# Optimization experiments

Hardware: AMD Instinct MI355X
Metric: run time of the kernel (lower is better)

Reference implementation:

```python
import jax, jax.numpy as jnp
import numpy as np

INPUT_SIZE = 2048
HIDDEN_SIZE = 4096
NUM_CLASSES = 1000
BATCH = 4096


def setup_inputs() -> dict:
    key = jax.random.key(0)
    kx, k1, k2, k3 = jax.random.split(key, 4)
    x = jax.random.normal(kx, (BATCH, INPUT_SIZE), dtype=jnp.float32)
    w1 = jax.random.normal(k1, (INPUT_SIZE, HIDDEN_SIZE), dtype=jnp.float32) * 0.01
    b1 = jnp.zeros((HIDDEN_SIZE,), dtype=jnp.float32)
    w2 = jax.random.normal(k2, (HIDDEN_SIZE, HIDDEN_SIZE), dtype=jnp.float32) * 0.01
    b2 = jnp.zeros((HIDDEN_SIZE,), dtype=jnp.float32)
    w3 = jax.random.normal(k3, (HIDDEN_SIZE, NUM_CLASSES), dtype=jnp.float32) * 0.01
    b3 = jnp.zeros((NUM_CLASSES,), dtype=jnp.float32)
    return {"x": x, "w1": w1, "b1": b1, "w2": w2, "b2": b2, "w3": w3, "b3": b3}


def reference(x, w1, b1, w2, b2, w3, b3):
    # fused GEMM + bias + ReLU, equivalent to the original Python double-loop matmul
    h1 = jax.nn.relu(x @ w1 + b1)    # [B, H]
    h2 = jax.nn.relu(h1 @ w2 + b2)   # [B, H]
    out = h2 @ w3 + b3               # [B, C]
    return out
```

## Files before the change

kernel.cpp:

```cpp
#include <hip/hip_runtime.h>
#include <hip/hip_bf16.h>

typedef __bf16 bf16x8 __attribute__((ext_vector_type(8)));
typedef __bf16 bf16x4 __attribute__((ext_vector_type(4)));
typedef float floatx4 __attribute__((ext_vector_type(4)));

#define B_    4096
#define IN_   2048
#define HID_  4096
#define NC_   1000
#define NCP_  1024

__device__ __forceinline__ void transpose_cvt_dev(const float* __restrict__ src,
                                                  __bf16* __restrict__ dst,
                                                  int R, int C, int bx, int by,
                                                  float* tile ) {
    const int r0 = bx * 64;
    const int c0 = by * 64;
    const int t  = threadIdx.x;
#pragma unroll
    for (int it = 0; it < 4; ++it) {
        int lin = it * 256 + t;
        int sr = lin >> 4, c4 = lin & 15;
        int cb = c0 + c4 * 4;
        const float* s = src + (size_t)(r0 + sr) * C;
        float4 v;
        if (cb + 3 < C) {
            v = *(const float4*)(s + cb);
        } else {
            v.x = (cb + 0 < C) ? s[cb + 0] : 0.f;
            v.y = (cb + 1 < C) ? s[cb + 1] : 0.f;
            v.z = (cb + 2 < C) ? s[cb + 2] : 0.f;
            v.w = (cb + 3 < C) ? s[cb + 3] : 0.f;
        }
        tile[(c4 * 4 + 0) * 65 + sr] = v.x;
        tile[(c4 * 4 + 1) * 65 + sr] = v.y;
        tile[(c4 * 4 + 2) * 65 + sr] = v.z;
        tile[(c4 * 4 + 3) * 65 + sr] = v.w;
    }
    __syncthreads();
#pragma unroll
    for (int it = 0; it < 2; ++it) {
        int lin = it * 256 + t;
        int dr = lin >> 3, q8 = lin & 7;
        bf16x8 o;
#pragma unroll
        for (int j = 0; j < 8; ++j) o[j] = (__bf16)tile[dr * 65 + q8 * 8 + j];
        *(bf16x8*)(dst + (size_t)(c0 + dr) * R + r0 + q8 * 8) = o;
    }
}

__device__ __forceinline__ void swizzle32x32(int bid, int& bx, int& by) {
    int xcd = bid & 7;
    int q   = bid >> 3;
    by = ((xcd >> 2) << 4) + (q & 15);
    bx = ((xcd & 3) << 3) + (q >> 4);
}

template <bool RELU, bool OUT_BF16>
__device__ __forceinline__ void gemm_core(const __bf16* __restrict__ A,
                                          const __bf16* __restrict__ Bt,
                                          const float* __restrict__ bias,
                                          void* __restrict__ Cv,
                                          int M, int K, int Nstore,
                                          int bx, int by,
                                          __bf16* sA, __bf16* sB) {
    const int tid   = threadIdx.x;
    const int lane  = tid & 63;
    const int wave  = tid >> 6;
    const int wr    = wave >> 1;
    const int wc    = wave & 1;
    const int mBase = by * 128;
    const int nBase = bx * 128;
    const int lr    = lane >> 4;
    const int lc    = lane & 15;

    floatx4 acc[4][4];
#pragma unroll
    for (int i = 0; i < 4; ++i)
#pragma unroll
        for (int j = 0; j < 4; ++j) acc[i][j] = (floatx4)0.f;

    for (int k0 = 0; k0 < K; k0 += 64) {
#pragma unroll
        for (int it = 0; it < 4; ++it) {
            int lin = it * 256 + tid;
            int r   = lin >> 3;
            int kc  = (lin & 7) ^ (r & 7);
            const __bf16* ga = A  + (size_t)(mBase + r) * K + k0 + kc * 8;
            const __bf16* gb = Bt + (size_t)(nBase + r) * K + k0 + kc * 8;
            __builtin_amdgcn_global_load_lds(
                (__attribute__((address_space(1))) void*)ga,
                (__attribute__((address_space(3))) void*)(sA + lin * 8), 16, 0, 0);
            __builtin_amdgcn_global_load_lds(
                (__attribute__((address_space(1))) void*)gb,
                (__attribute__((address_space(3))) void*)(sB + lin * 8), 16, 0, 0);
        }
        __builtin_amdgcn_s_waitcnt(0);
        __syncthreads();

#pragma unroll
        for (int kk = 0; kk < 2; ++kk) {
            const int sw = (kk * 4 + lr) ^ (lc & 7);
            bf16x8 af[4], bfr[4];
#pragma unroll
            for (int i = 0; i < 4; ++i)
                af[i] = *(const bf16x8*)(sA + (wr * 64 + i * 16 + lc) * 64 + sw * 8);
#pragma unroll
            for (int j = 0; j < 4; ++j)
                bfr[j] = *(const bf16x8*)(sB + (wc * 64 + j * 16 + lc) * 64 + sw * 8);
#pragma unroll
            for (int i = 0; i < 4; ++i)
#pragma unroll
                for (int j = 0; j < 4; ++j)
                    acc[i][j] = __builtin_amdgcn_mfma_f32_16x16x32_bf16(af[i], bfr[j], acc[i][j], 0, 0, 0);
        }
        __syncthreads();
    }

#pragma unroll
    for (int j = 0; j < 4; ++j) {
        int col = nBase + wc * 64 + j * 16 + lc;
        if (col < Nstore) {
            float bv = bias[col];
#pragma unroll
            for (int i = 0; i < 4; ++i) {
                int rowb = mBase + wr * 64 + i * 16 + lr * 4;
#pragma unroll
                for (int r = 0; r < 4; ++r) {
                    float v = acc[i][j][r] + bv;
                    if (RELU) v = fmaxf(v, 0.f);
                    if (OUT_BF16)
                        ((__bf16*)Cv)[(size_t)(rowb + r) * Nstore + col] = (__bf16)v;
                    else
                        ((float*)Cv)[(size_t)(rowb + r) * Nstore + col] = v;
                }
            }
        }
    }
}

__global__ __launch_bounds__(256) void prep1(const float* __restrict__ x,
                                             __bf16* __restrict__ xb,
                                             const float* __restrict__ w1,
                                             __bf16* __restrict__ w1t) {
    __shared__ float tile[64 * 65];
    const int b = blockIdx.x;
    if (b < 4096) {
        int i = (b * 256 + (int)threadIdx.x) * 8;
        float4 a = *(const float4*)(x + i);
        float4 c = *(const float4*)(x + i + 4);
        bf16x8 o;
        o[0] = (__bf16)a.x; o[1] = (__bf16)a.y; o[2] = (__bf16)a.z; o[3] = (__bf16)a.w;
        o[4] = (__bf16)c.x; o[5] = (__bf16)c.y; o[6] = (__bf16)c.z; o[7] = (__bf16)c.w;
        *(bf16x8*)(xb + i) = o;
    } else {
        int l = b - 4096;
        transpose_cvt_dev(w1, w1t, IN_, HID_, l & 31, l >> 5, tile);
    }
}

__global__ __launch_bounds__(256, 2) void gemm1_fused(const __bf16* __restrict__ xb,
                                                      const __bf16* __restrict__ w1t,
                                                      const float* __restrict__ b1,
                                                      __bf16* __restrict__ h1,
                                                      const float* __restrict__ w2,
                                                      __bf16* __restrict__ w2t,
                                                      const float* __restrict__ w3,
                                                      __bf16* __restrict__ w3t) {
    __shared__ float smem[8192];
    const int b = blockIdx.x;
    if (b < 1024) {
        __bf16* sA = (__bf16*)smem;
        __bf16* sB = sA + 128 * 64;
        int bx, by;
        swizzle32x32(b, bx, by);
        gemm_core<true, true>(xb, w1t, b1, h1, B_, IN_, HID_, bx, by, sA, sB);
    } else if (b < 5120) {
        int l = b - 1024;
        transpose_cvt_dev(w2, w2t, HID_, HID_, l & 63, l >> 6, smem);
    } else {
        int l = b - 5120;
        transpose_cvt_dev(w3, w3t, HID_, NC_, l & 63, l >> 6, smem);
    }
}

#define QPHASE(pA, pB, qm, qn, ...)                                            \
  {                                                                            \
    bf16x8 af0[4], af1[4], bq0[2], bq1[2];                                     \
    _Pragma("unroll") for (int i_ = 0; i_ < 4; ++i_) {                         \
      const __bf16* ap_ = (pA) + ((wr * 128 + (qm) * 64 + i_ * 16 + lc) * 64); \
      af0[i_] = *(const bf16x8*)(ap_ + ((0 + lr) ^ (lc & 7)) * 8);             \
      af1[i_] = *(const bf16x8*)(ap_ + ((4 + lr) ^ (lc & 7)) * 8);             \
    }                                                                          \
    _Pragma("unroll") for (int j_ = 0; j_ < 2; ++j_) {                         \
      const __bf16* bp_ = (pB) + ((wc * 64 + (qn) * 32 + j_ * 16 + lc) * 64);  \
      bq0[j_] = *(const bf16x8*)(bp_ + ((0 + lr) ^ (lc & 7)) * 8);             \
      bq1[j_] = *(const bf16x8*)(bp_ + ((4 + lr) ^ (lc & 7)) * 8);             \
    }                                                                          \
    __VA_ARGS__;                                                               \
    __builtin_amdgcn_s_barrier();                                              \
    asm volatile("s_waitcnt lgkmcnt(0)" ::: "memory");                         \
    __builtin_amdgcn_sched_barrier(0);                                         \
    __builtin_amdgcn_s_setprio(1);                                             \
    _Pragma("unroll") for (int i_ = 0; i_ < 4; ++i_)                           \
      _Pragma("unroll") for (int j_ = 0; j_ < 2; ++j_) {                       \
        acc[(qm) * 4 + i_][(qn) * 2 + j_] =                                    \
            __builtin_amdgcn_mfma_f32_16x16x32_bf16(                           \
                af0[i_], bq0[j_], acc[(qm) * 4 + i_][(qn) * 2 + j_], 0, 0, 0); \
        acc[(qm) * 4 + i_][(qn) * 2 + j_] =                                    \
            __builtin_amdgcn_mfma_f32_16x16x32_bf16(                           \
                af1[i_], bq1[j_], acc[(qm) * 4 + i_][(qn) * 2 + j_], 0, 0, 0); \
      }                                                                        \
    __builtin_amdgcn_s_setprio(0);                                             \
    __builtin_amdgcn_s_barrier();                                              \
  }

__global__ __launch_bounds__(512, 2) void gemm2_256(const __bf16* __restrict__ A,
                                                    const __bf16* __restrict__ Bt,
                                                    const float* __restrict__ bias,
                                                    __bf16* __restrict__ C) {
    extern __shared__ __bf16 lds[];
    const int K  = HID_;
    const int NT = K / 64;

    const int tid  = threadIdx.x;
    const int lane = tid & 63;
    const int wave = tid >> 6;
    const int wr   = wave >> 2;
    const int wc   = wave & 3;
    const int lr   = lane >> 4;
    const int lc   = lane & 15;

    int bid = blockIdx.y * 16 + blockIdx.x;
    int xcd = bid & 7, q = bid >> 3;
    const int by = (xcd & 3) * 4 + (q & 3);
    const int bx = (xcd >> 2) * 8 + (q >> 2);
    const int mBase = by * 256;
    const int nBase = bx * 256;

    __bf16* A0buf = lds;
    __bf16* B0buf = lds + 16384;
    __bf16* A1buf = lds + 32768;
    __bf16* B1buf = lds + 49152;

    auto stage_half = [&](const __bf16* __restrict__ src, int rowBase, int k0,
                          __bf16* dst) {
#pragma unroll
        for (int it = 0; it < 2; ++it) {
            int lin = it * 512 + tid;
            int rl  = lin >> 3;
            int kc  = (lin & 7) ^ (rl & 7);
            const __bf16* gp = src + (size_t)(rowBase + rl) * HID_ + k0 + kc * 8;
            __builtin_amdgcn_global_load_lds(
                (__attribute__((address_space(1))) void*)gp,
                (__attribute__((address_space(3))) void*)(dst + lin * 8), 16, 0, 0);
        }
    };

    floatx4 acc[8][4];
#pragma unroll
    for (int i = 0; i < 8; ++i)
#pragma unroll
        for (int j = 0; j < 4; ++j) acc[i][j] = (floatx4)0.f;

    stage_half(A,  mBase,       0,  A0buf);
    stage_half(A,  mBase + 128, 0,  A0buf + 8192);
    stage_half(Bt, nBase,       0,  B0buf);
    stage_half(Bt, nBase + 128, 0,  B0buf + 8192);
    stage_half(A,  mBase,       64, A1buf);
    stage_half(A,  mBase + 128, 64, A1buf + 8192);
    asm volatile("s_waitcnt vmcnt(4)" ::: "memory");
    __builtin_amdgcn_s_barrier();

    for (int t = 0; t < NT; t += 2) {
        QPHASE(A0buf, B0buf, 0, 0, stage_half(Bt, nBase,       (t + 1) * 64, B1buf));
        QPHASE(A0buf, B0buf, 0, 1, stage_half(Bt, nBase + 128, (t + 1) * 64, B1buf + 8192));
        QPHASE(A0buf, B0buf, 1, 0, );
        QPHASE(A0buf, B0buf, 1, 1, );
        if (t + 2 < NT) {
            stage_half(A, mBase,       (t + 2) * 64, A0buf);
            stage_half(A, mBase + 128, (t + 2) * 64, A0buf + 8192);
            asm volatile("s_waitcnt vmcnt(4)" ::: "memory");
        } else {
            asm volatile("s_waitcnt vmcnt(0)" ::: "memory");
        }
        __builtin_amdgcn_s_barrier();

        QPHASE(A1buf, B1buf, 0, 0, if (t + 2 < NT) stage_half(Bt, nBase,       (t + 2) * 64, B0buf));
        QPHASE(A1buf, B1buf, 0, 1, if (t + 2 < NT) stage_half(Bt, nBase + 128, (t + 2) * 64, B0buf + 8192));
        QPHASE(A1buf, B1buf, 1, 0, );
        QPHASE(A1buf, B1buf, 1, 1, );
        if (t + 3 < NT) {
            stage_half(A, mBase,       (t + 3) * 64, A1buf);
            stage_half(A, mBase + 128, (t + 3) * 64, A1buf + 8192);
            asm volatile("s_waitcnt vmcnt(4)" ::: "memory");
        } else {
            asm volatile("s_waitcnt vmcnt(0)" ::: "memory");
        }
        __builtin_amdgcn_s_barrier();
    }

#pragma unroll
    for (int n = 0; n < 4; ++n) {
        int col = nBase + wc * 64 + n * 16 + lc;
        float bv = bias[col];
#pragma unroll
        for (int m = 0; m < 8; ++m) {
            int rowb = mBase + wr * 128 + m * 16 + lr * 4;
#pragma unroll
            for (int r = 0; r < 4; ++r) {
                float v = fmaxf(acc[m][n][r] + bv, 0.f);
                C[(size_t)(rowb + r) * HID_ + col] = (__bf16)v;
            }
        }
    }
}

__global__ __launch_bounds__(256, 2) void gemm_sk(const __bf16* __restrict__ A,
                                                  const __bf16* __restrict__ Bt,
                                                  float* __restrict__ P,
                                                  int M, int KH, int Ktot) {
    __shared__ __bf16 sA[128 * 64];
    __shared__ __bf16 sB[128 * 64];

    const int tid   = threadIdx.x;
    const int lane  = tid & 63;
    const int wave  = tid >> 6;
    const int wr    = wave >> 1;
    const int wc    = wave & 1;
    const int mBase = blockIdx.y * 128;
    const int nBase = blockIdx.x * 128;
    const int z     = blockIdx.z;
    const int kOff  = z * KH;
    const int lr    = lane >> 4;
    const int lc    = lane & 15;

    floatx4 acc[4][4];
#pragma unroll
    for (int i = 0; i < 4; ++i)
#pragma unroll
        for (int j = 0; j < 4; ++j) acc[i][j] = (floatx4)0.f;

    for (int k0 = kOff; k0 < kOff + KH; k0 += 64) {
#pragma unroll
        for (int it = 0; it < 4; ++it) {
            int lin = it * 256 + tid;
            int r   = lin >> 3;
            int kc  = (lin & 7) ^ (r & 7);
            const __bf16* ga = A  + (size_t)(mBase + r) * Ktot + k0 + kc * 8;
            const __bf16* gb = Bt + (size_t)(nBase + r) * Ktot + k0 + kc * 8;
            __builtin_amdgcn_global_load_lds(
                (__attribute__((address_space(1))) void*)ga,
                (__attribute__((address_space(3))) void*)(sA + lin * 8), 16, 0, 0);
            __builtin_amdgcn_global_load_lds(
                (__attribute__((address_space(1))) void*)gb,
                (__attribute__((address_space(3))) void*)(sB + lin * 8), 16, 0, 0);
        }
        __builtin_amdgcn_s_waitcnt(0);
        __syncthreads();

#pragma unroll
        for (int kk = 0; kk < 2; ++kk) {
            const int sw = (kk * 4 + lr) ^ (lc & 7);
            bf16x8 af[4], bfr[4];
#pragma unroll
            for (int i = 0; i < 4; ++i)
                af[i] = *(const bf16x8*)(sA + (wr * 64 + i * 16 + lc) * 64 + sw * 8);
#pragma unroll
            for (int j = 0; j < 4; ++j)
                bfr[j] = *(const bf16x8*)(sB + (wc * 64 + j * 16 + lc) * 64 + sw * 8);
#pragma unroll
            for (int i = 0; i < 4; ++i)
#pragma unroll
                for (int j = 0; j < 4; ++j)
                    acc[i][j] = __builtin_amdgcn_mfma_f32_16x16x32_bf16(af[i], bfr[j], acc[i][j], 0, 0, 0);
        }
        __syncthreads();
    }

    float* Pz = P + (size_t)z * M * NCP_;
#pragma unroll
    for (int j = 0; j < 4; ++j) {
        int col = nBase + wc * 64 + j * 16 + lc;
#pragma unroll
        for (int i = 0; i < 4; ++i) {
            int rowb = mBase + wr * 64 + i * 16 + lr * 4;
#pragma unroll
            for (int r = 0; r < 4; ++r)
                Pz[(size_t)(rowb + r) * NCP_ + col] = acc[i][j][r];
        }
    }
}

__global__ __launch_bounds__(256) void reduce_bias(const float* __restrict__ P,
                                                   const float* __restrict__ b3,
                                                   float* __restrict__ out) {
    int c = blockIdx.x * 256 + threadIdx.x;
    int m = blockIdx.y;
    if (c < NC_)
        out[(size_t)m * NC_ + c] =
            P[(size_t)m * NCP_ + c] + P[(size_t)(B_ + m) * NCP_ + c] + b3[c];
}

extern "C" void kernel_launch(void* const* d_in, const int* in_sizes, int n_in,
                              void* d_out, int out_size, void* d_ws, size_t ws_size,
                              hipStream_t stream) {
    const float* x  = (const float*)d_in[0];
    const float* w1 = (const float*)d_in[1];
    const float* b1 = (const float*)d_in[2];
    const float* w2 = (const float*)d_in[3];
    const float* b2 = (const float*)d_in[4];
    const float* w3 = (const float*)d_in[5];
    const float* b3 = (const float*)d_in[6];
    float* out = (float*)d_out;

    char* ws = (char*)d_ws;
    __bf16* xb  = (__bf16*)(ws);
    __bf16* w1t = (__bf16*)(ws + (16u << 20));
    __bf16* w2t = (__bf16*)(ws + (32u << 20));
    __bf16* w3t = (__bf16*)(ws + (64u << 20));
    __bf16* h1  = (__bf16*)(ws + (72u << 20));
    __bf16* h2  = (__bf16*)(ws);
    float*  P   = (float*)(ws + (72u << 20));

    static int attr_done = 0;
    if (!attr_done) {
        (void)hipFuncSetAttribute((const void*)gemm2_256,
                                  hipFuncAttributeMaxDynamicSharedMemorySize,
                                  131072);
        attr_done = 1;
    }

    prep1<<<6144, 256, 0, stream>>>(x, xb, w1, w1t);

    gemm1_fused<<<6144, 256, 0, stream>>>(xb, w1t, b1, h1, w2, w2t, w3, w3t);

    gemm2_256<<<dim3(16, 16), 512, 131072, stream>>>(h1, w2t, b2, h2);

    gemm_sk<<<dim3(NCP_ / 128, B_ / 128, 2), 256, 0, stream>>>(
        h2, w3t, P, B_, HID_ / 2, HID_);
    reduce_bias<<<dim3(NCP_ / 256, B_), 256, 0, stream>>>(P, b3, out);
}
```

Measured before the change: 453.6 us.

## Restructure GEMM2 inner loop to load B once per tile and pipeline A fragments

The hidden-layer GEMM inner loop is reorganized so each wave reads its B fragments from LDS once per K-tile, not twice across quadrant phases. A fragments are ping-ponged in two register sets and loaded ahead of the MFMAs that consume them, with partial lgkmcnt waits. The intent is to cut redundant LDS reads and hide LDS latency behind MFMA work. It raises register pressure under the 2-blocks-per-CU launch bound, and the barrier placement changes.

```diff
diff --git a/kernel.cpp b/kernel.cpp
--- a/kernel.cpp
+++ b/kernel.cpp
@@ -185,44 +185,68 @@
     }
 }
 
-#define QPHASE(pA, pB, qm, qn, ...)                                            \
-  {                                                                            \
-    bf16x8 af0[4], af1[4], bq0[2], bq1[2];                                     \
-    _Pragma("unroll") for (int i_ = 0; i_ < 4; ++i_) {                         \
-      const __bf16* ap_ = (pA) + ((wr * 128 + (qm) * 64 + i_ * 16 + lc) * 64); \
-      af0[i_] = *(const bf16x8*)(ap_ + ((0 + lr) ^ (lc & 7)) * 8);             \
-      af1[i_] = *(const bf16x8*)(ap_ + ((4 + lr) ^ (lc & 7)) * 8);             \
-    }                                                                          \
-    _Pragma("unroll") for (int j_ = 0; j_ < 2; ++j_) {                         \
-      const __bf16* bp_ = (pB) + ((wc * 64 + (qn) * 32 + j_ * 16 + lc) * 64);  \
-      bq0[j_] = *(const bf16x8*)(bp_ + ((0 + lr) ^ (lc & 7)) * 8);             \
-      bq1[j_] = *(const bf16x8*)(bp_ + ((4 + lr) ^ (lc & 7)) * 8);             \
-    }                                                                          \
+#define BAR() __builtin_amdgcn_s_barrier()
+#define LGKM(n)                                                  \
+    asm volatile("s_waitcnt lgkmcnt(" #n ")" ::: "memory");      \
+    __builtin_amdgcn_sched_barrier(0)
+#define VMCNT(n) asm volatile("s_waitcnt vmcnt(" #n ")" ::: "memory")
+
+#define LDA2(dst, mb, pA)                                                      \
+    _Pragma("unroll") for (int mi_ = 0; mi_ < 2; ++mi_)                        \
+    _Pragma("unroll") for (int kk_ = 0; kk_ < 2; ++kk_)                        \
+        dst[mi_][kk_] = *(const bf16x8*)((pA) +                                \
+            (wr * 128 + ((mb) + mi_) * 16 + lc) * 64 +                         \
+            (((kk_ * 4) + lr) ^ (lc & 7)) * 8);
+
+#define LDB8(pB)                                                               \
+    _Pragma("unroll") for (int n_ = 0; n_ < 4; ++n_)                           \
+    _Pragma("unroll") for (int kk_ = 0; kk_ < 2; ++kk_)                        \
+        bq[n_][kk_] = *(const bf16x8*)((pB) +                                  \
+            (wc * 64 + n_ * 16 + lc) * 64 +                                    \
+            (((kk_ * 4) + lr) ^ (lc & 7)) * 8);
+
+#define MFMA16(aset, mb)                                                       \
+    _Pragma("unroll") for (int mi_ = 0; mi_ < 2; ++mi_)                        \
+    _Pragma("unroll") for (int n_ = 0; n_ < 4; ++n_) {                         \
+        acc[(mb) + mi_][n_] = __builtin_amdgcn_mfma_f32_16x16x32_bf16(         \
+            aset[mi_][0], bq[n_][0], acc[(mb) + mi_][n_], 0, 0, 0);            \
+        acc[(mb) + mi_][n_] = __builtin_amdgcn_mfma_f32_16x16x32_bf16(         \
+            aset[mi_][1], bq[n_][1], acc[(mb) + mi_][n_], 0, 0, 0);            \
+    }
+
+#define DO_TILE(base, S0, S1, ...) {                                           \
+    const __bf16* pA_ = (base);                                                \
+    const __bf16* pB_ = (base) + 16384;                                        \
+    bf16x8 bq[4][2], aX[2][2], aY[2][2];                                       \
+    LDB8(pB_);                                                                 \
+    LDA2(aX, 0, pA_);                                                          \
+    LDA2(aY, 2, pA_);                                                          \
+    S0;                                                                        \
+    BAR(); LGKM(4);                                                            \
+    __builtin_amdgcn_s_setprio(1); MFMA16(aX, 0); __builtin_amdgcn_s_setprio(0); \
+    BAR();                                                                     \
+    LDA2(aX, 4, pA_);                                                          \
+    S1;                                                                        \
+    BAR(); LGKM(4);                                                            \
+    __builtin_amdgcn_s_setprio(1); MFMA16(aY, 2); __builtin_amdgcn_s_setprio(0); \
+    BAR();                                                                     \
+    LDA2(aY, 6, pA_);                                                          \
+    BAR(); LGKM(4);                                                            \
+    __builtin_amdgcn_s_setprio(1); MFMA16(aX, 4); __builtin_amdgcn_s_setprio(0); \
+    BAR();                                                                     \
+    LGKM(0);                                                                   \
+    __builtin_amdgcn_s_setprio(1); MFMA16(aY, 6); __builtin_amdgcn_s_setprio(0); \
+    BAR();                                                                     \
     __VA_ARGS__;                                                               \
-    __builtin_amdgcn_s_barrier();                                              \
-    asm volatile("s_waitcnt lgkmcnt(0)" ::: "memory");                         \
-    __builtin_amdgcn_sched_barrier(0);                                         \
-    __builtin_amdgcn_s_setprio(1);                                             \
-    _Pragma("unroll") for (int i_ = 0; i_ < 4; ++i_)                           \
-      _Pragma("unroll") for (int j_ = 0; j_ < 2; ++j_) {                       \
-        acc[(qm) * 4 + i_][(qn) * 2 + j_] =                                    \
-            __builtin_amdgcn_mfma_f32_16x16x32_bf16(                           \
-                af0[i_], bq0[j_], acc[(qm) * 4 + i_][(qn) * 2 + j_], 0, 0, 0); \
-        acc[(qm) * 4 + i_][(qn) * 2 + j_] =                                    \
-            __builtin_amdgcn_mfma_f32_16x16x32_bf16(                           \
-                af1[i_], bq1[j_], acc[(qm) * 4 + i_][(qn) * 2 + j_], 0, 0, 0); \
-      }                                                                        \
-    __builtin_amdgcn_s_setprio(0);                                             \
-    __builtin_amdgcn_s_barrier();                                              \
-  }
+    BAR();                                                                     \
+}
 
 __global__ __launch_bounds__(512, 2) void gemm2_256(const __bf16* __restrict__ A,
                                                     const __bf16* __restrict__ Bt,
                                                     const float* __restrict__ bias,
                                                     __bf16* __restrict__ C) {
     extern __shared__ __bf16 lds[];
-    const int K  = HID_;
-    const int NT = K / 64;
+    const int NT = HID_ / 64;
 
     const int tid  = threadIdx.x;
     const int lane = tid & 63;
@@ -238,11 +262,6 @@
     const int bx = (xcd >> 2) * 8 + (q >> 2);
     const int mBase = by * 256;
     const int nBase = bx * 256;
-
-    __bf16* A0buf = lds;
-    __bf16* B0buf = lds + 16384;
-    __bf16* A1buf = lds + 32768;
-    __bf16* B1buf = lds + 49152;
 
     auto stage_half = [&](const __bf16* __restrict__ src, int rowBase, int k0,
                           __bf16* dst) {
@@ -264,41 +283,36 @@
 #pragma unroll
         for (int j = 0; j < 4; ++j) acc[i][j] = (floatx4)0.f;
 
-    stage_half(A,  mBase,       0,  A0buf);
-    stage_half(A,  mBase + 128, 0,  A0buf + 8192);
-    stage_half(Bt, nBase,       0,  B0buf);
-    stage_half(Bt, nBase + 128, 0,  B0buf + 8192);
-    stage_half(A,  mBase,       64, A1buf);
-    stage_half(A,  mBase + 128, 64, A1buf + 8192);
-    asm volatile("s_waitcnt vmcnt(4)" ::: "memory");
-    __builtin_amdgcn_s_barrier();
+    stage_half(A,  mBase,       0,  lds);
+    stage_half(A,  mBase + 128, 0,  lds + 8192);
+    stage_half(Bt, nBase,       0,  lds + 16384);
+    stage_half(Bt, nBase + 128, 0,  lds + 16384 + 8192);
+    stage_half(A,  mBase,       64, lds + 32768);
+    stage_half(A,  mBase + 128, 64, lds + 32768 + 8192);
+    VMCNT(4);
+    BAR();
 
     for (int t = 0; t < NT; t += 2) {
-        QPHASE(A0buf, B0buf, 0, 0, stage_half(Bt, nBase,       (t + 1) * 64, B1buf));
-        QPHASE(A0buf, B0buf, 0, 1, stage_half(Bt, nBase + 128, (t + 1) * 64, B1buf + 8192));
-        QPHASE(A0buf, B0buf, 1, 0, );
-        QPHASE(A0buf, B0buf, 1, 1, );
-        if (t + 2 < NT) {
-            stage_half(A, mBase,       (t + 2) * 64, A0buf);
-            stage_half(A, mBase + 128, (t + 2) * 64, A0buf + 8192);
-            asm volatile("s_waitcnt vmcnt(4)" ::: "memory");
-        } else {
-            asm volatile("s_waitcnt vmcnt(0)" ::: "memory");
-        }
-        __builtin_amdgcn_s_barrier();
-
-        QPHASE(A1buf, B1buf, 0, 0, if (t + 2 < NT) stage_half(Bt, nBase,       (t + 2) * 64, B0buf));
-        QPHASE(A1buf, B1buf, 0, 1, if (t + 2 < NT) stage_half(Bt, nBase + 128, (t + 2) * 64, B0buf + 8192));
-        QPHASE(A1buf, B1buf, 1, 0, );
-        QPHASE(A1buf, B1buf, 1, 1, );
-        if (t + 3 < NT) {
-            stage_half(A, mBase,       (t + 3) * 64, A1buf);
-            stage_half(A, mBase + 128, (t + 3) * 64, A1buf + 8192);
-            asm volatile("s_waitcnt vmcnt(4)" ::: "memory");
-        } else {
-            asm volatile("s_waitcnt vmcnt(0)" ::: "memory");
-        }
-        __builtin_amdgcn_s_barrier();
+        DO_TILE(lds,
+                stage_half(Bt, nBase,       (t + 1) * 64, lds + 49152),
+                stage_half(Bt, nBase + 128, (t + 1) * 64, lds + 49152 + 8192),
+                if (t + 2 < NT) {
+                    stage_half(A, mBase,       (t + 2) * 64, lds);
+                    stage_half(A, mBase + 128, (t + 2) * 64, lds + 8192);
+                    VMCNT(4);
+                } else {
+                    VMCNT(0);
+                });
+        DO_TILE(lds + 32768,
+                if (t + 2 < NT) stage_half(Bt, nBase,       (t + 2) * 64, lds + 16384),
+                if (t + 2 < NT) stage_half(Bt, nBase + 128, (t + 2) * 64, lds + 16384 + 8192),
+                if (t + 3 < NT) {
+                    stage_half(A, mBase,       (t + 3) * 64, lds + 32768);
+                    stage_half(A, mBase + 128, (t + 3) * 64, lds + 32768 + 8192);
+                    VMCNT(4);
+                } else {
+                    VMCNT(0);
+                });
     }
 
 #pragma unroll
```

Measured after the change: 428.8 us. 5.5% less time.
